# Kernel tuning notes

Measured on AMD Instinct MI355X. Metric: run time of the kernel, lower is better.

The kernel has to match this reference:

```python
import jax, jax.numpy as jnp
import numpy as np

NBITS = 4
GROUP = 128
K = 4096   # in_features
N = 4096   # out_features
M = 4096   # flattened batch*seq tokens
EPS = 32 // NBITS  # elements per packed int32 = 8
MASK = (1 << NBITS) - 1  # unpack_mask = 15


def setup_inputs() -> dict:
    key = jax.random.key(0)
    k1, k2, k3, k4, k5 = jax.random.split(key, 5)
    x = jax.random.normal(k1, (M, K), dtype=jnp.float32)
    # raw 4-bit quantized weights, layout [K, N] (i.e. W_q.t() from the torch module)
    nib = jax.random.randint(k2, (K, N), 0, 1 << NBITS, dtype=jnp.int32)
    # pack EPS nibbles per int32 along K, matching pack(): element j gets shift j*NBITS
    nib = nib.reshape(K // EPS, EPS, N)
    shifts = (jnp.arange(EPS, dtype=jnp.int32) * NBITS)[None, :, None]
    parts = nib << shifts  # disjoint bit ranges
    W_q_packed = parts[:, 0]
    for j in range(1, EPS):
        W_q_packed = W_q_packed | parts[:, j]
    W_q_packed = W_q_packed.astype(jnp.int32)  # [K//EPS, N]
    # group-wise scales/zeros: [K//GROUP, N] (scales.view(N,-1).t() layout)
    scales = (jax.random.uniform(k3, (K // GROUP, N), dtype=jnp.float32) + 0.5) * 0.01
    zeros = jax.random.uniform(k4, (K // GROUP, N), dtype=jnp.float32) * MASK
    bias = jax.random.normal(k5, (N,), dtype=jnp.float32) * 0.1
    return {"x": x, "W_q_packed": W_q_packed, "scales": scales, "zeros": zeros, "bias": bias}


def reference(x, W_q_packed, scales, zeros, bias):
    # unpack: w[k, n] = (packed[k//EPS, n] >> ((k % EPS) * NBITS)) & MASK
    shifts = (jnp.arange(EPS, dtype=jnp.int32) * NBITS)[None, :, None]
    w = (W_q_packed[:, None, :] >> shifts) & MASK  # [K//EPS, EPS, N]
    w = w.reshape(K, N).astype(jnp.float32)
    # group-wise asymmetric dequant (W_group_mode == 3): W = (w - z) * s
    s = jnp.repeat(scales, GROUP, axis=0)  # [K, N]
    z = jnp.repeat(zeros, GROUP, axis=0)   # [K, N]
    W = (w - z) * s
    out = x @ W + bias  # [M, N]
    return out
```

## Files before the change

### kernel.cpp

```cpp
#include <hip/hip_runtime.h>
#include <stdint.h>


#define M_DIM 4096
#define N_DIM 4096
#define K_DIM 4096
#define NT (K_DIM / 64)

typedef __attribute__((ext_vector_type(8))) short short8;
typedef __attribute__((ext_vector_type(4))) float f32x4;

__device__ __forceinline__ unsigned short f2bf(float f) {
  uint32_t u = __builtin_bit_cast(uint32_t, f);
  u += 0x7fffu + ((u >> 16) & 1u);
  return (unsigned short)(u >> 16);
}

__global__ __launch_bounds__(256) void prep_kernel(const float* __restrict__ x,
                                                   unsigned short* __restrict__ xb,
                                                   const int* __restrict__ Wq,
                                                   const float* __restrict__ scales,
                                                   const float* __restrict__ zeros,
                                                   unsigned short* __restrict__ wt) {
  __shared__ uint4 Ts[32 * 64];
  const int tid = threadIdx.x;
  if (blockIdx.x < 2048) {
    const int total = (M_DIM * K_DIM) / 8;
    const float4* x4 = (const float4*)x;
    uint4* o8 = (uint4*)xb;
#pragma unroll
    for (int p = 0; p < 4; ++p) {
      int i = (p * 2048 + blockIdx.x) * 256 + tid;
      if (i < total) {
        float4 a = x4[2 * i], b = x4[2 * i + 1];
        uint4 o;
        o.x = (uint32_t)f2bf(a.x) | ((uint32_t)f2bf(a.y) << 16);
        o.y = (uint32_t)f2bf(a.z) | ((uint32_t)f2bf(a.w) << 16);
        o.z = (uint32_t)f2bf(b.x) | ((uint32_t)f2bf(b.y) << 16);
        o.w = (uint32_t)f2bf(b.z) | ((uint32_t)f2bf(b.w) << 16);
        o8[i] = o;
      }
    }
    return;
  }
  const int blk = blockIdx.x - 2048;
  const int n0 = (blk & 127) * 32;
  const int gk0 = (blk >> 7) * 64;

#pragma unroll
  for (int p = 0; p < 8; ++p) {
    int e = p * 256 + tid;
    int n_l = e & 31;
    int gk_l = e >> 5;
    int gk = gk0 + gk_l;
    int n = n0 + n_l;
    int g = gk >> 4;
    uint32_t q = (uint32_t)Wq[gk * N_DIM + n];
    float s = scales[g * N_DIM + n];
    float z = zeros[g * N_DIM + n];
    unsigned short b[8];
#pragma unroll
    for (int j = 0; j < 8; ++j) {
      float f = ((float)((q >> (4 * j)) & 15u) - z) * s;
      b[j] = f2bf(f);
    }
    uint4 cell;
    cell.x = (uint32_t)b[0] | ((uint32_t)b[1] << 16);
    cell.y = (uint32_t)b[2] | ((uint32_t)b[3] << 16);
    cell.z = (uint32_t)b[4] | ((uint32_t)b[5] << 16);
    cell.w = (uint32_t)b[6] | ((uint32_t)b[7] << 16);
    Ts[n_l * 64 + (gk_l ^ (n_l & 7))] = cell;
  }
  __syncthreads();
  uint4* dst = (uint4*)wt;
#pragma unroll
  for (int p = 0; p < 8; ++p) {
    int n_l = p * 4 + (tid >> 6);
    int gk_l = tid & 63;
    uint4 cell = Ts[n_l * 64 + (gk_l ^ (n_l & 7))];
    dst[(size_t)(n0 + n_l) * (K_DIM / 8) + (gk0 + gk_l)] = cell;
  }
}


#define STAGEH(DST, SRC)                                                        \
  {                                                                             \
    __builtin_amdgcn_global_load_lds(                                           \
        (const __attribute__((address_space(1))) void*)(SRC),                   \
        (__attribute__((address_space(3))) void*)((DST) + tid), 16, 0, 0);      \
    __builtin_amdgcn_global_load_lds(                                           \
        (const __attribute__((address_space(1))) void*)((SRC) + 64 * K_DIM),    \
        (__attribute__((address_space(3))) void*)((DST) + tid + 512), 16, 0, 0);\
  }

#define LOADAF(RB)                                                              \
  {                                                                             \
    _Pragma("unroll") for (int mi = 0; mi < 4; ++mi) {                          \
      af[mi][0] = ASb[(RB)*1024 + a_base + mi * 128 + kx0];                     \
      af[mi][1] = ASb[(RB)*1024 + a_base + mi * 128 + kx1];                     \
    }                                                                           \
  }

#define LOADBV(CB)                                                              \
  {                                                                             \
    _Pragma("unroll") for (int ni = 0; ni < 2; ++ni) {                          \
      bv[ni][0] = BSb[(CB)*1024 + b_base + ni * 128 + kx0];                     \
      bv[ni][1] = BSb[(CB)*1024 + b_base + ni * 128 + kx1];                     \
    }                                                                           \
  }

#define MFMAQ(RB, CB)                                                           \
  {                                                                             \
    __builtin_amdgcn_s_setprio(1);                                              \
    _Pragma("unroll") for (int mi = 0; mi < 4; ++mi)                            \
        _Pragma("unroll") for (int ni = 0; ni < 2; ++ni) {                      \
      acc[(RB)*4 + mi][(CB)*2 + ni] = __builtin_amdgcn_mfma_f32_16x16x32_bf16(  \
          af[mi][0], bv[ni][0], acc[(RB)*4 + mi][(CB)*2 + ni], 0, 0, 0);        \
      acc[(RB)*4 + mi][(CB)*2 + ni] = __builtin_amdgcn_mfma_f32_16x16x32_bf16(  \
          af[mi][1], bv[ni][1], acc[(RB)*4 + mi][(CB)*2 + ni], 0, 0, 0);        \
    }                                                                           \
    __builtin_amdgcn_s_setprio(0);                                              \
  }

#define WAIT_VM6                                           \
  asm volatile("s_waitcnt vmcnt(6)" ::: "memory");         \
  __builtin_amdgcn_sched_barrier(0);

#define WAIT_LGKM0                                         \
  asm volatile("s_waitcnt lgkmcnt(0)" ::: "memory");       \
  __builtin_amdgcn_sched_barrier(0);

__global__ __launch_bounds__(512, 2) void gemm_bt_kernel(
    const unsigned short* __restrict__ A, const unsigned short* __restrict__ Bt,
    const float* __restrict__ bias, float* __restrict__ C) {
  __shared__ short8 As[2 * 2048];
  __shared__ short8 Bs[2 * 2048];

  const int tid = threadIdx.x;
  const int lane = tid & 63;
  const int w = tid >> 6;
  const int wm = w >> 2;
  const int wn = w & 3;

  const int b = blockIdx.x;
  const int xcd = b & 7;
  const int loc = b >> 3;
  const int nt = xcd * 2 + (loc & 1);
  const int mt = loc >> 1;
  const int m0 = mt * 256;
  const int n0 = nt * 256;

  const int srow = tid >> 3;
  const int skc = (tid & 7) ^ (srow & 7);
  const unsigned short* Asrc0 = A + (size_t)(m0 + srow) * K_DIM + skc * 8;
  const unsigned short* Asrc1 = Asrc0 + (size_t)128 * K_DIM;
  const unsigned short* Bsrc0 = Bt + (size_t)(n0 + srow) * K_DIM + skc * 8;
  const unsigned short* Bsrc1 = Bsrc0 + (size_t)128 * K_DIM;

  const int fr = lane & 15;
  const int fc = lane >> 4;
  const int frx = fr & 7;
  const int a_base = (wm * 64 + fr) * 8;
  const int b_base = (wn * 32 + fr) * 8;
  const int kx0 = fc ^ frx;
  const int kx1 = (4 + fc) ^ frx;

  f32x4 acc[8][4] = {};
  short8 af[4][2];
  short8 bv[2][2];

  STAGEH(As, Asrc0);
  STAGEH(Bs, Bsrc0);
  STAGEH(Bs + 1024, Bsrc1);
  STAGEH(As + 1024, Asrc1);
  STAGEH(As + 2048, Asrc0 + 64);
  STAGEH(Bs + 2048, Bsrc0 + 64);
  asm volatile("s_waitcnt vmcnt(8)" ::: "memory");
  __builtin_amdgcn_sched_barrier(0);
  __builtin_amdgcn_s_barrier();

  for (int kt = 0; kt < NT; ++kt) {
    const int cur = kt & 1;
    const short8* ASb = As + cur * 2048;
    const short8* BSb = Bs + cur * 2048;
    short8* Anx = As + (cur ^ 1) * 2048;
    short8* Bnx = Bs + (cur ^ 1) * 2048;
    short8* Asame = As + cur * 2048;
    short8* Bsame = Bs + cur * 2048;
    const bool p1ok = (kt + 1 < NT);
    const bool p2ok = (kt + 2 < NT);

    WAIT_VM6;
    LOADAF(0);
    LOADBV(0);
    if (p1ok) STAGEH(Bnx + 1024, Bsrc1 + (size_t)(kt + 1) * 64);
    __builtin_amdgcn_s_barrier();
    WAIT_LGKM0;
    MFMAQ(0, 0);
    __builtin_amdgcn_s_barrier();

    WAIT_VM6;
    LOADBV(1);
    if (p1ok) STAGEH(Anx + 1024, Asrc1 + (size_t)(kt + 1) * 64);
    __builtin_amdgcn_s_barrier();
    WAIT_LGKM0;
    MFMAQ(0, 1);
    __builtin_amdgcn_s_barrier();

    WAIT_VM6;
    LOADAF(1);
    LOADBV(0);
    if (p2ok) STAGEH(Asame, Asrc0 + (size_t)(kt + 2) * 64);
    __builtin_amdgcn_s_barrier();
    WAIT_LGKM0;
    MFMAQ(1, 0);
    __builtin_amdgcn_s_barrier();

    WAIT_VM6;
    LOADBV(1);
    if (p2ok) STAGEH(Bsame, Bsrc0 + (size_t)(kt + 2) * 64);
    __builtin_amdgcn_s_barrier();
    WAIT_LGKM0;
    MFMAQ(1, 1);
    __builtin_amdgcn_s_barrier();
  }

  const int rr = (lane >> 4) * 4;
#pragma unroll
  for (int cb = 0; cb < 2; ++cb)
#pragma unroll
    for (int ni = 0; ni < 2; ++ni) {
      const int gn = n0 + cb * 128 + wn * 32 + ni * 16 + fr;
      const float bvv = bias[gn];
#pragma unroll
      for (int rb = 0; rb < 2; ++rb)
#pragma unroll
        for (int mi = 0; mi < 4; ++mi) {
          const int gm = m0 + rb * 128 + wm * 64 + mi * 16 + rr;
#pragma unroll
          for (int r = 0; r < 4; ++r)
            C[(size_t)(gm + r) * N_DIM + gn] = acc[rb * 4 + mi][cb * 2 + ni][r] + bvv;
        }
    }
}

extern "C" void kernel_launch(void* const* d_in, const int* in_sizes, int n_in,
                              void* d_out, int out_size, void* d_ws, size_t ws_size,
                              hipStream_t stream) {
  const float* x = (const float*)d_in[0];
  const int* wq = (const int*)d_in[1];
  const float* sc = (const float*)d_in[2];
  const float* zr = (const float*)d_in[3];
  const float* bias = (const float*)d_in[4];
  float* out = (float*)d_out;

  unsigned short* xb = (unsigned short*)d_ws;
  unsigned short* wt = (unsigned short*)((char*)d_ws + (size_t)M_DIM * K_DIM * 2);

  prep_kernel<<<dim3(3072), dim3(256), 0, stream>>>(x, xb, wq, sc, zr, wt);
  gemm_bt_kernel<<<dim3(256), dim3(512), 0, stream>>>(xb, wt, bias, out);
}
```

Measured before the change: 262.9 us.

## Restructure GEMM prefetch schedule with peeled tail iterations and reordered MFMA quadrants

Rewrites the main K-loop of the bf16 GEMM so each k-tile runs four MFMA quadrants in a new order (00, 01, 11, 10). Global-to-LDS stages are prefetched two tiles ahead for three of the four half-tiles, and B's first half is staged only one tile ahead. A single vmcnt wait moves to the end of each tile instead of four per tile. The last two tiles are peeled out of the loop, which removes the per-iteration guard predicates. The aim is fewer waits and better overlap of memory traffic with MFMA work, at the cost of a more intricate buffer-reuse scheme with a risk of LDS hazards.

Result: no change. 260.2 us (-1.0%).

```diff
diff --git a/kernel.cpp b/kernel.cpp
--- a/kernel.cpp
+++ b/kernel.cpp
@@ -122,13 +122,53 @@
     __builtin_amdgcn_s_setprio(0);                                              \
   }
 
-#define WAIT_VM6                                           \
-  asm volatile("s_waitcnt vmcnt(6)" ::: "memory");         \
-  __builtin_amdgcn_sched_barrier(0);
-
 #define WAIT_LGKM0                                         \
   asm volatile("s_waitcnt lgkmcnt(0)" ::: "memory");       \
   __builtin_amdgcn_sched_barrier(0);
+
+#define EW6                                                \
+  asm volatile("s_waitcnt vmcnt(6)" ::: "memory");         \
+  __builtin_amdgcn_sched_barrier(0)
+
+#define EW0                                                \
+  asm volatile("s_waitcnt vmcnt(0)" ::: "memory");         \
+  __builtin_amdgcn_sched_barrier(0)
+
+#define KTILE(S1, S2, S3, S4, EW)                          \
+  {                                                        \
+                            \
+    LOADAF(0);                                             \
+    LOADBV(0);                                             \
+    S1;                                                    \
+    asm volatile("s_waitcnt lgkmcnt(8)" ::: "memory");     \
+    __builtin_amdgcn_sched_barrier(0);                     \
+    __builtin_amdgcn_s_barrier();                          \
+    WAIT_LGKM0;                                            \
+    MFMAQ(0, 0);                                           \
+    __builtin_amdgcn_s_barrier();                          \
+                    \
+    LOADBV(1);                                             \
+    S2;                                                    \
+    __builtin_amdgcn_s_barrier();                          \
+    WAIT_LGKM0;                                            \
+    MFMAQ(0, 1);                                           \
+    __builtin_amdgcn_s_barrier();                          \
+                    \
+    LOADAF(1);                                             \
+    S3;                                                    \
+    __builtin_amdgcn_s_barrier();                          \
+    WAIT_LGKM0;                                            \
+    MFMAQ(1, 1);                                           \
+    __builtin_amdgcn_s_barrier();                          \
+     \
+    LOADBV(0);                                             \
+    S4;                                                    \
+    __builtin_amdgcn_s_barrier();                          \
+    WAIT_LGKM0;                                            \
+    MFMAQ(1, 0);                                           \
+    EW;                                                    \
+    __builtin_amdgcn_s_barrier();                          \
+  }
 
 __global__ __launch_bounds__(512, 2) void gemm_bt_kernel(
     const unsigned short* __restrict__ A, const unsigned short* __restrict__ Bt,
@@ -174,55 +214,41 @@
   STAGEH(Bs + 1024, Bsrc1);
   STAGEH(As + 1024, Asrc1);
   STAGEH(As + 2048, Asrc0 + 64);
-  STAGEH(Bs + 2048, Bsrc0 + 64);
-  asm volatile("s_waitcnt vmcnt(8)" ::: "memory");
-  __builtin_amdgcn_sched_barrier(0);
+  STAGEH(Bs + 3072, Bsrc1 + 64);
+  STAGEH(As + 3072, Asrc1 + 64);
+  EW6;
   __builtin_amdgcn_s_barrier();
 
-  for (int kt = 0; kt < NT; ++kt) {
+  for (int kt = 0; kt < NT - 2; ++kt) {
     const int cur = kt & 1;
     const short8* ASb = As + cur * 2048;
     const short8* BSb = Bs + cur * 2048;
-    short8* Anx = As + (cur ^ 1) * 2048;
-    short8* Bnx = Bs + (cur ^ 1) * 2048;
-    short8* Asame = As + cur * 2048;
-    short8* Bsame = Bs + cur * 2048;
-    const bool p1ok = (kt + 1 < NT);
-    const bool p2ok = (kt + 2 < NT);
-
-    WAIT_VM6;
-    LOADAF(0);
-    LOADBV(0);
-    if (p1ok) STAGEH(Bnx + 1024, Bsrc1 + (size_t)(kt + 1) * 64);
-    __builtin_amdgcn_s_barrier();
-    WAIT_LGKM0;
-    MFMAQ(0, 0);
-    __builtin_amdgcn_s_barrier();
-
-    WAIT_VM6;
-    LOADBV(1);
-    if (p1ok) STAGEH(Anx + 1024, Asrc1 + (size_t)(kt + 1) * 64);
-    __builtin_amdgcn_s_barrier();
-    WAIT_LGKM0;
-    MFMAQ(0, 1);
-    __builtin_amdgcn_s_barrier();
-
-    WAIT_VM6;
-    LOADAF(1);
-    LOADBV(0);
-    if (p2ok) STAGEH(Asame, Asrc0 + (size_t)(kt + 2) * 64);
-    __builtin_amdgcn_s_barrier();
-    WAIT_LGKM0;
-    MFMAQ(1, 0);
-    __builtin_amdgcn_s_barrier();
-
-    WAIT_VM6;
-    LOADBV(1);
-    if (p2ok) STAGEH(Bsame, Bsrc0 + (size_t)(kt + 2) * 64);
-    __builtin_amdgcn_s_barrier();
-    WAIT_LGKM0;
-    MFMAQ(1, 1);
-    __builtin_amdgcn_s_barrier();
+    short8* Adst0 = As + cur * 2048;
+    short8* Adst1 = As + cur * 2048 + 1024;
+    short8* Bdst0 = Bs + ((kt + 1) & 1) * 2048;
+    short8* Bdst1 = Bs + cur * 2048 + 1024;
+    const size_t k1 = (size_t)(kt + 1) * 64;
+    const size_t k2 = (size_t)(kt + 2) * 64;
+
+    KTILE(STAGEH(Bdst0, Bsrc0 + k1),
+          STAGEH(Adst0, Asrc0 + k2),
+          STAGEH(Bdst1, Bsrc1 + k2),
+          STAGEH(Adst1, Asrc1 + k2),
+          EW6);
+  }
+
+  {
+    const short8* ASb = As;
+    const short8* BSb = Bs;
+    short8* Bdst0 = Bs + 2048;
+    const size_t k1 = (size_t)(NT - 1) * 64;
+    KTILE(STAGEH(Bdst0, Bsrc0 + k1), (void)0, (void)0, (void)0, EW0);
+  }
+
+  {
+    const short8* ASb = As + 2048;
+    const short8* BSb = Bs + 2048;
+    KTILE((void)0, (void)0, (void)0, (void)0, (void)0);
   }
 
   const int rr = (lane >> 4) * 4;
```
